# Optimization experiments

Hardware: AMD Instinct MI355X
Metric: run time of the kernel (lower is better)

Reference implementation:

```python
import jax, jax.numpy as jnp
import numpy as np

EMBED_DIM = 1024
NUM_HEADS = 16
HEAD_DIM = EMBED_DIM // NUM_HEADS
B, N = 4, 2048


def setup_inputs() -> dict:
    key = jax.random.key(0)
    k = jax.random.split(key, 5)
    s = 1.0 / np.sqrt(EMBED_DIM)
    return {
        "x": jax.random.normal(k[0], (B, N, EMBED_DIM), dtype=jnp.float32),
        "W_qkv": jax.random.uniform(k[1], (EMBED_DIM, 3 * EMBED_DIM), jnp.float32, -s, s),
        "b_qkv": jax.random.uniform(k[2], (3 * EMBED_DIM,), jnp.float32, -s, s),
        "W_proj": jax.random.uniform(k[3], (EMBED_DIM, EMBED_DIM), jnp.float32, -s, s),
        "b_proj": jax.random.uniform(k[4], (EMBED_DIM,), jnp.float32, -s, s),
    }


def reference(x, W_qkv, b_qkv, W_proj, b_proj):
    b, n, c = x.shape
    qkv = x @ W_qkv + b_qkv                       # [B,N,3C]
    qkv = qkv.reshape(b, n, 3, NUM_HEADS, HEAD_DIM)
    q = qkv[:, :, 0].transpose(0, 2, 1, 3)        # [B,H,N,D]
    k = qkv[:, :, 1].transpose(0, 2, 1, 3)
    v = qkv[:, :, 2].transpose(0, 2, 1, 3)
    scale = 1.0 / np.sqrt(HEAD_DIM).astype(np.float32)
    scores = jnp.einsum("bhqd,bhkd->bhqk", q, k) * scale
    attn = jax.nn.softmax(scores, axis=-1)
    out = jnp.einsum("bhqk,bhkd->bhqd", attn, v)  # [B,H,N,D]
    out = out.transpose(0, 2, 1, 3).reshape(b, n, c)
    return out @ W_proj + b_proj
```

## Files before the change

### kernel.cpp

```cpp
#include <hip/hip_runtime.h>
#include <math.h>


typedef __bf16 bf16x8 __attribute__((ext_vector_type(8)));
typedef float f32x4 __attribute__((ext_vector_type(4)));

#define EMBED 1024
#define NHEAD 16
#define BATCH 4
#define SEQ 2048
#define M_TOT 8192
#define QKV_N 3072
#define QSCALE 0.18033688011112042f

__device__ __forceinline__ ushort f2bf(float f) {
  union { float f; unsigned u; } x; x.f = f;
  unsigned r = x.u + 0x7FFFu + ((x.u >> 16) & 1u);
  return (ushort)(r >> 16);
}

__device__ __forceinline__ uint cvt2bf(float a, float b) {
#if __has_builtin(__builtin_amdgcn_cvt_pk_bf16_f32)
  typedef __bf16 bf16x2 __attribute__((ext_vector_type(2)));
  union { bf16x2 v; uint u; } c;
  c.v = __builtin_amdgcn_cvt_pk_bf16_f32(a, b);
  return c.u;
#else
  return (uint)f2bf(a) | ((uint)f2bf(b) << 16);
#endif
}

__device__ __forceinline__ float fexp2(float x) {
#if __has_builtin(__builtin_amdgcn_exp2f)
  return __builtin_amdgcn_exp2f(x);
#else
  return exp2f(x);
#endif
}

__device__ __forceinline__ f32x4 mfma16(bf16x8 a, bf16x8 b, f32x4 c) {
  return __builtin_amdgcn_mfma_f32_16x16x32_bf16(a, b, c, 0, 0, 0);
}

__device__ __forceinline__ void gl2lds16(const void* g, void* l) {
  __builtin_amdgcn_global_load_lds(
      (const __attribute__((address_space(1))) unsigned int*)g,
      (__attribute__((address_space(3))) unsigned int*)l, 16, 0, 0);
}

__global__ __launch_bounds__(256) void prep_kernel(
    const float* __restrict__ x, ushort* __restrict__ xb,
    const float* __restrict__ Wqkv, ushort* __restrict__ Wqkv_t,
    const float* __restrict__ Wproj, ushort* __restrict__ Wproj_t) {
  __shared__ float tile[64][65];
  const int bid = blockIdx.x;
  const int t = threadIdx.x;
  if (bid < 8192) {
    int i = (bid * 256 + t) * 4;
    float4 v = *reinterpret_cast<const float4*>(&x[i]);
    uint2 w = {cvt2bf(v.x, v.y), cvt2bf(v.z, v.w)};
    *reinterpret_cast<uint2*>(&xb[i]) = w;
    return;
  }
  const float* in;
  ushort* out;
  int Kd = 1024, Nd, n0, k0;
  if (bid < 8960) {
    int b2 = bid - 8192;
    in = Wqkv; out = Wqkv_t; Nd = 3072;
    n0 = (b2 % 48) * 64; k0 = (b2 / 48) * 64;
  } else {
    int b2 = bid - 8960;
    in = Wproj; out = Wproj_t; Nd = 1024;
    n0 = (b2 % 16) * 64; k0 = (b2 / 16) * 64;
  }
#pragma unroll
  for (int i = 0; i < 16; ++i) {
    int e = t + 256 * i;
    int kr = e >> 6, nc = e & 63;
    tile[kr][nc] = in[(size_t)(k0 + kr) * Nd + n0 + nc];
  }
  __syncthreads();
#pragma unroll
  for (int i = 0; i < 16; ++i) {
    int e = t + 256 * i;
    int nr = e >> 6, kc = e & 63;
    out[(size_t)(n0 + nr) * Kd + k0 + kc] = f2bf(tile[kc][nr]);
  }
}

__global__ __launch_bounds__(512, 4) void gemm_bf16(
    const ushort* __restrict__ A, const ushort* __restrict__ Bt,
    const float* __restrict__ bias, void* __restrict__ Cout,
    ushort* __restrict__ vtgout, int M, int N, int K, int mode) {
  __shared__ ushort As[2][128 * 32];
  __shared__ ushort Bs[2][128 * 32];
  const int t = threadIdx.x;
  const int wave = t >> 6, lane = t & 63;
  const int lane15 = lane & 15, quad = lane >> 4;
  const int m0 = blockIdx.y * 128, n0 = blockIdx.x * 128;
  const int wm = (wave >> 2) * 64, wn = (wave & 3) * 32;

  const int srow = t >> 2;
  const int scol = ((t & 3) ^ ((srow >> 1) & 3)) * 8;
  const int sdst = wave * 512;
  const ushort* ap = &A[(size_t)(m0 + srow) * K + scol];
  const ushort* bp = &Bt[(size_t)(n0 + srow) * K + scol];

  const int sw2 = (lane15 >> 1) & 3;

  f32x4 acc[4][2] = {};

  const int NIT = K >> 5;
  gl2lds16(ap, &As[0][sdst]);
  gl2lds16(bp, &Bs[0][sdst]);
  __syncthreads();

  for (int kt = 0; kt < NIT; ++kt) {
    const int cur = kt & 1, nxt = cur ^ 1;
    if (kt < NIT - 1) {
      gl2lds16(ap + (kt + 1) * 32, &As[nxt][sdst]);
      gl2lds16(bp + (kt + 1) * 32, &Bs[nxt][sdst]);
    }

    bf16x8 af[4], bfr[2];
#pragma unroll
    for (int ms = 0; ms < 4; ++ms)
      af[ms] = *reinterpret_cast<const bf16x8*>(
          &As[cur][(wm + ms * 16 + lane15) * 32 + ((quad ^ sw2) * 8)]);
#pragma unroll
    for (int ns = 0; ns < 2; ++ns)
      bfr[ns] = *reinterpret_cast<const bf16x8*>(
          &Bs[cur][(wn + ns * 16 + lane15) * 32 + ((quad ^ sw2) * 8)]);
#pragma unroll
    for (int ms = 0; ms < 4; ++ms)
#pragma unroll
      for (int ns = 0; ns < 2; ++ns)
        acc[ms][ns] = mfma16(af[ms], bfr[ns], acc[ms][ns]);

    __syncthreads();
  }

  if (mode == 0) {
    float* out = (float*)Cout;
#pragma unroll
    for (int ns = 0; ns < 2; ++ns) {
      int col = n0 + wn + ns * 16 + lane15;
      float bv = bias[col];
#pragma unroll
      for (int ms = 0; ms < 4; ++ms)
#pragma unroll
        for (int r = 0; r < 4; ++r) {
          int row = m0 + wm + ms * 16 + quad * 4 + r;
          out[(size_t)row * N + col] = acc[ms][ns][r] + bv;
        }
    }
  } else {
    ushort* qk = (ushort*)Cout;
#pragma unroll
    for (int ns = 0; ns < 2; ++ns) {
      int col = n0 + wn + ns * 16 + lane15;
      float bv = bias[col];
      if (col < 2048) {
        float sc = (col < 1024) ? QSCALE : 1.0f;
#pragma unroll
        for (int ms = 0; ms < 4; ++ms) {
          int row = m0 + wm + ms * 16 + quad * 4;
          uint u01 = cvt2bf((acc[ms][ns][0] + bv) * sc, (acc[ms][ns][1] + bv) * sc);
          uint u23 = cvt2bf((acc[ms][ns][2] + bv) * sc, (acc[ms][ns][3] + bv) * sc);
          qk[(size_t)(row + 0) * 2048 + col] = (ushort)u01;
          qk[(size_t)(row + 1) * 2048 + col] = (ushort)(u01 >> 16);
          qk[(size_t)(row + 2) * 2048 + col] = (ushort)u23;
          qk[(size_t)(row + 3) * 2048 + col] = (ushort)(u23 >> 16);
        }
      } else {
        int dp = col - 2048;
#pragma unroll
        for (int ms = 0; ms < 4; ++ms) {
          int row = m0 + wm + ms * 16 + quad * 4;
          int b = row >> 11, seq = row & 2047;
          uint2 w = {cvt2bf(acc[ms][ns][0] + bv, acc[ms][ns][1] + bv),
                     cvt2bf(acc[ms][ns][2] + bv, acc[ms][ns][3] + bv)};
          *reinterpret_cast<uint2*>(
              &vtgout[((size_t)(b * 1024 + dp) << 11) + seq]) = w;
        }
      }
    }
  }
}

#define QG 2

__global__ __launch_bounds__(256, 4) void attn_kernel(
    const ushort* __restrict__ qk, const ushort* __restrict__ vtg,
    ushort* __restrict__ out) {
  __shared__ ushort Ks[2][4096];
  __shared__ ushort Vt[2][4096];
  __shared__ ushort Ps[4][16 * 64];

  const int t = threadIdx.x;
  const int wave = t >> 6, lane = t & 63;
  const int lane15 = lane & 15, quad = lane >> 4;
  const int bh = blockIdx.x, qg = blockIdx.y;
  const int b = bh >> 4, h = bh & 15;
  const size_t boff = (size_t)b * SEQ * 2048;

  int sdst[2];
  const ushort* kptr[2];
  const ushort* vptr[2];
#pragma unroll
  for (int j = 0; j < 2; ++j) {
    int lg = (j * 4 + wave) * 64 + lane;
    int row = lg >> 3;
    int col = ((lg & 7) ^ (row & 7)) * 8;
    sdst[j] = (j * 4 + wave) * 512;
    kptr[j] = qk + boff + (size_t)row * 2048 + 1024 + h * 64 + col;
    vptr[j] = vtg + ((size_t)(b * 1024 + h * 64 + row) << 11) + col;
  }

  bf16x8 qf[QG][2];
#pragma unroll
  for (int g = 0; g < QG; ++g) {
    size_t qoff = boff +
        (size_t)(qg * (QG * 64) + g * 64 + wave * 16 + lane15) * 2048 + h * 64;
    qf[g][0] = *reinterpret_cast<const bf16x8*>(&qk[qoff + quad * 8]);
    qf[g][1] = *reinterpret_cast<const bf16x8*>(&qk[qoff + 32 + quad * 8]);
  }

  bf16x8 ones;
#pragma unroll
  for (int j = 0; j < 8; ++j) ones[j] = (__bf16)1.0f;

  f32x4 O[QG][4] = {};
  f32x4 lacc[QG] = {};
  const int sw = lane15 & 7;
  ushort* ps = Ps[wave];

#pragma unroll
  for (int j = 0; j < 2; ++j) {
    gl2lds16(kptr[j], &Ks[0][sdst[j]]);
    gl2lds16(vptr[j], &Vt[0][sdst[j]]);
  }
  __syncthreads();

  for (int kt = 0; kt < SEQ / 64; ++kt) {
    const int cur = kt & 1, nxt = cur ^ 1;
    if (kt < SEQ / 64 - 1) {
#pragma unroll
      for (int j = 0; j < 2; ++j) {
        gl2lds16(kptr[j] + (size_t)(kt + 1) * 64 * 2048, &Ks[nxt][sdst[j]]);
        gl2lds16(vptr[j] + (kt + 1) * 64, &Vt[nxt][sdst[j]]);
      }
    }

    bf16x8 kf[4][2], vf[2][4];
#pragma unroll
    for (int nsub = 0; nsub < 4; ++nsub) {
      const int kr = (nsub * 16 + lane15) * 64;
      kf[nsub][0] = *reinterpret_cast<const bf16x8*>(
          &Ks[cur][kr + ((quad ^ sw) * 8)]);
      kf[nsub][1] = *reinterpret_cast<const bf16x8*>(
          &Ks[cur][kr + (((quad + 4) ^ sw) * 8)]);
    }
#pragma unroll
    for (int kk = 0; kk < 2; ++kk)
#pragma unroll
      for (int dsub = 0; dsub < 4; ++dsub) {
        int d = dsub * 16 + lane15;
        vf[kk][dsub] = *reinterpret_cast<const bf16x8*>(
            &Vt[cur][d * 64 + (((kk * 4 + quad) ^ sw) * 8)]);
      }

#pragma unroll
    for (int g = 0; g < QG; ++g) {
      f32x4 st[4];
#pragma unroll
      for (int nsub = 0; nsub < 4; ++nsub) {
        f32x4 a = {-32.0f, -32.0f, -32.0f, -32.0f};
        a = mfma16(kf[nsub][0], qf[g][0], a);
        a = mfma16(kf[nsub][1], qf[g][1], a);
        st[nsub] = a;
      }
#pragma unroll
      for (int nsub = 0; nsub < 4; ++nsub) {
        uint2 w = {cvt2bf(fexp2(st[nsub][0]), fexp2(st[nsub][1])),
                   cvt2bf(fexp2(st[nsub][2]), fexp2(st[nsub][3]))};
        *reinterpret_cast<uint2*>(
            &ps[lane15 * 64 + (((2 * nsub + (quad >> 1)) ^ sw) << 3) +
                ((quad & 1) << 2)]) = w;
      }
#pragma unroll
      for (int kk = 0; kk < 2; ++kk) {
        bf16x8 pf = *reinterpret_cast<const bf16x8*>(
            &ps[lane15 * 64 + (((kk * 4 + quad) ^ sw) << 3)]);
#pragma unroll
        for (int dsub = 0; dsub < 4; ++dsub)
          O[g][dsub] = mfma16(pf, vf[kk][dsub], O[g][dsub]);
        lacc[g] = mfma16(pf, ones, lacc[g]);
      }
    }
    __syncthreads();
  }

#pragma unroll
  for (int g = 0; g < QG; ++g)
#pragma unroll
    for (int r = 0; r < 4; ++r) {
      float linv = __builtin_amdgcn_rcpf(lacc[g][r]);
      size_t rowoff =
          (size_t)(b * SEQ + qg * (QG * 64) + g * 64 + wave * 16 + quad * 4 +
                   r) * EMBED + h * 64;
      uint u01 = cvt2bf(O[g][0][r] * linv, O[g][1][r] * linv);
      uint u23 = cvt2bf(O[g][2][r] * linv, O[g][3][r] * linv);
      out[rowoff + 0 * 16 + lane15] = (ushort)u01;
      out[rowoff + 1 * 16 + lane15] = (ushort)(u01 >> 16);
      out[rowoff + 2 * 16 + lane15] = (ushort)u23;
      out[rowoff + 3 * 16 + lane15] = (ushort)(u23 >> 16);
    }
}

extern "C" void kernel_launch(void* const* d_in, const int* in_sizes, int n_in,
                              void* d_out, int out_size, void* d_ws,
                              size_t ws_size, hipStream_t stream) {
  const float* x = (const float*)d_in[0];
  const float* Wqkv = (const float*)d_in[1];
  const float* bqkv = (const float*)d_in[2];
  const float* Wproj = (const float*)d_in[3];
  const float* bproj = (const float*)d_in[4];
  float* out = (float*)d_out;

  char* ws = (char*)d_ws;
  ushort* Wqkv_t = (ushort*)ws;
  ushort* Wproj_t = (ushort*)(ws + 6291456);
  ushort* qk = (ushort*)(ws + 8388608);
  ushort* vtg = (ushort*)(ws + 41943040);
  ushort* xb = (ushort*)(ws + 58720256);
  ushort* attnout = (ushort*)(ws + 58720256);

  prep_kernel<<<8192 + 768 + 256, 256, 0, stream>>>(
      x, xb, Wqkv, Wqkv_t, Wproj, Wproj_t);
  gemm_bf16<<<dim3(QKV_N / 128, M_TOT / 128), 512, 0, stream>>>(
      xb, Wqkv_t, bqkv, qk, vtg, M_TOT, QKV_N, EMBED, 1);
  attn_kernel<<<dim3(NHEAD * BATCH, SEQ / (QG * 64)), 256, 0, stream>>>(
      qk, vtg, attnout);
  gemm_bf16<<<dim3(EMBED / 128, M_TOT / 128), 512, 0, stream>>>(
      attnout, Wproj_t, bproj, out, nullptr, M_TOT, EMBED, EMBED, 0);
}
```

Before: 293.5 us.

## Deepen GEMM LDS pipeline to four stages with explicit vmcnt waits

Replaces the double-buffered GEMM main loop with a four-buffer ring that keeps three K-tiles of global-to-LDS loads in flight. Each iteration uses `s_waitcnt vmcnt` to wait only for the oldest tile, then a single barrier, instead of waiting on every load and syncing at the loop end. The aim is to hide global memory latency behind MFMA work. In exchange, LDS per block doubles to 64KB, which can limit how many blocks fit on a CU. The hand-counted vmcnt values also rely on each `gl2lds16` call issuing exactly one memory instruction.

```diff
diff --git a/kernel.cpp b/kernel.cpp
--- a/kernel.cpp
+++ b/kernel.cpp
@@ -93,8 +93,8 @@
     const ushort* __restrict__ A, const ushort* __restrict__ Bt,
     const float* __restrict__ bias, void* __restrict__ Cout,
     ushort* __restrict__ vtgout, int M, int N, int K, int mode) {
-  __shared__ ushort As[2][128 * 32];
-  __shared__ ushort Bs[2][128 * 32];
+  __shared__ ushort As[4][4096];
+  __shared__ ushort Bs[4][4096];
   const int t = threadIdx.x;
   const int wave = t >> 6, lane = t & 63;
   const int lane15 = lane & 15, quad = lane >> 4;
@@ -112,34 +112,49 @@
   f32x4 acc[4][2] = {};
 
   const int NIT = K >> 5;
-  gl2lds16(ap, &As[0][sdst]);
-  gl2lds16(bp, &Bs[0][sdst]);
-  __syncthreads();
-
-  for (int kt = 0; kt < NIT; ++kt) {
-    const int cur = kt & 1, nxt = cur ^ 1;
-    if (kt < NIT - 1) {
-      gl2lds16(ap + (kt + 1) * 32, &As[nxt][sdst]);
-      gl2lds16(bp + (kt + 1) * 32, &Bs[nxt][sdst]);
-    }
-
+
+  auto step = [&](int bi) {
     bf16x8 af[4], bfr[2];
 #pragma unroll
     for (int ms = 0; ms < 4; ++ms)
       af[ms] = *reinterpret_cast<const bf16x8*>(
-          &As[cur][(wm + ms * 16 + lane15) * 32 + ((quad ^ sw2) * 8)]);
+          &As[bi][(wm + ms * 16 + lane15) * 32 + ((quad ^ sw2) * 8)]);
 #pragma unroll
     for (int ns = 0; ns < 2; ++ns)
       bfr[ns] = *reinterpret_cast<const bf16x8*>(
-          &Bs[cur][(wn + ns * 16 + lane15) * 32 + ((quad ^ sw2) * 8)]);
+          &Bs[bi][(wn + ns * 16 + lane15) * 32 + ((quad ^ sw2) * 8)]);
 #pragma unroll
     for (int ms = 0; ms < 4; ++ms)
 #pragma unroll
       for (int ns = 0; ns < 2; ++ns)
         acc[ms][ns] = mfma16(af[ms], bfr[ns], acc[ms][ns]);
-
-    __syncthreads();
-  }
+  };
+
+#pragma unroll
+  for (int j = 0; j < 3; ++j) {
+    gl2lds16(ap + j * 32, &As[j][sdst]);
+    gl2lds16(bp + j * 32, &Bs[j][sdst]);
+  }
+
+  for (int kt = 0; kt < NIT - 2; ++kt) {
+    asm volatile("s_waitcnt vmcnt(4)" ::: "memory");
+    __builtin_amdgcn_s_barrier();
+    __builtin_amdgcn_sched_barrier(0);
+    if (kt <= NIT - 4) {
+      int bs = (kt + 3) & 3;
+      gl2lds16(ap + (kt + 3) * 32, &As[bs][sdst]);
+      gl2lds16(bp + (kt + 3) * 32, &Bs[bs][sdst]);
+    }
+    step(kt & 3);
+  }
+  asm volatile("s_waitcnt vmcnt(2)" ::: "memory");
+  __builtin_amdgcn_s_barrier();
+  __builtin_amdgcn_sched_barrier(0);
+  step((NIT - 2) & 3);
+  asm volatile("s_waitcnt vmcnt(0)" ::: "memory");
+  __builtin_amdgcn_s_barrier();
+  __builtin_amdgcn_sched_barrier(0);
+  step((NIT - 1) & 3);
 
   if (mode == 0) {
     float* out = (float*)Cout;
```

Measured after the change: 296.7 us. Within noise of the previous version (+1.1%).
